# Kernel optimization log

Hardware: AMD Instinct MI355X
Metric: run time of the kernel (lower is better)

Reference implementation:

```python
import jax, jax.numpy as jnp
import numpy as np

EPS = 1e-5
TOPK = 2
SHARED_RATIO = 0.1

B, S, H = 2, 1024, 2048
NH, DH, R = 16, 128, 64
CQ, CKV = 1024, 512
E, I, NS = 8, 1024, 2


def rmsnorm(x, w):
    return x * jax.lax.rsqrt(jnp.mean(x * x, axis=-1, keepdims=True) + EPS) * w


def rope_cos_sin(seq_len, dim):
    inv = 1.0 / (10000.0 ** (jnp.arange(0, dim, 2, dtype=jnp.float32) / dim))
    t = jnp.arange(seq_len, dtype=jnp.float32)[:, None] * inv[None, :]  # [S, dim/2]
    return jnp.cos(t), jnp.sin(t)


def apply_rope(x, cos, sin):
    # rotate-half on last dim; cos/sin broadcast over leading dims
    x1, x2 = jnp.split(x, 2, axis=-1)
    return jnp.concatenate([x1 * cos - x2 * sin, x2 * cos + x1 * sin], axis=-1)


def swiglu(x, w1, w3, w2):
    return (jax.nn.silu(x @ w1) * (x @ w3)) @ w2


def setup_inputs() -> dict:
    key = jax.random.key(0)
    ks = jax.random.split(key, 24)
    sc = 0.02
    d = {
        'x': jax.random.normal(ks[0], (B, S, H), jnp.float32),
        'attn_norm_w': jnp.ones((H,), jnp.float32),
        'ffn_norm_w': jnp.ones((H,), jnp.float32),
        'W_dq': sc * jax.random.normal(ks[1], (H, CQ), jnp.float32),
        'q_norm_w': jnp.ones((CQ,), jnp.float32),
        'W_uq': sc * jax.random.normal(ks[2], (CQ, NH * DH), jnp.float32),
        'W_qr': sc * jax.random.normal(ks[3], (CQ, NH * R), jnp.float32),
        'W_dkv': sc * jax.random.normal(ks[4], (H, CKV), jnp.float32),
        'kv_norm_w': jnp.ones((CKV,), jnp.float32),
        'W_uk': sc * jax.random.normal(ks[5], (CKV, NH * DH), jnp.float32),
        'W_uv': sc * jax.random.normal(ks[6], (CKV, NH * DH), jnp.float32),
        'W_kr': sc * jax.random.normal(ks[7], (H, R), jnp.float32),
        'W_o': sc * jax.random.normal(ks[8], (NH * DH, H), jnp.float32),
        'centroids': sc * jax.random.normal(ks[9], (E, H), jnp.float32),
        'expert_bias': jnp.zeros((E,), jnp.float32),
        'w1': sc * jax.random.normal(ks[10], (E, H, I), jnp.float32),
        'w3': sc * jax.random.normal(ks[11], (E, H, I), jnp.float32),
        'w2': sc * jax.random.normal(ks[12], (E, I, H), jnp.float32),
        'w1s': sc * jax.random.normal(ks[13], (NS, H, I), jnp.float32),
        'w3s': sc * jax.random.normal(ks[14], (NS, H, I), jnp.float32),
        'w2s': sc * jax.random.normal(ks[15], (NS, I, H), jnp.float32),
    }
    return d


def reference(x, attn_norm_w, ffn_norm_w, W_dq, q_norm_w, W_uq, W_qr, W_dkv,
              kv_norm_w, W_uk, W_uv, W_kr, W_o, centroids, expert_bias,
              w1, w3, w2, w1s, w3s, w2s):
    b, s, h = x.shape
    r = W_kr.shape[1]
    nh = W_qr.shape[1] // r
    dh = W_uq.shape[1] // nh

    # ---- MLA attention (pre-norm) ----
    hn = rmsnorm(x, attn_norm_w)
    cq = rmsnorm(hn @ W_dq, q_norm_w)                    # [b,s,CQ] compressed query latent
    q = (cq @ W_uq).reshape(b, s, nh, dh)                # content queries
    qr = (cq @ W_qr).reshape(b, s, nh, r)                # rope queries
    ckv = rmsnorm(hn @ W_dkv, kv_norm_w)                 # [b,s,CKV] compressed kv latent
    k = (ckv @ W_uk).reshape(b, s, nh, dh)
    v = (ckv @ W_uv).reshape(b, s, nh, dh)
    kr = hn @ W_kr                                       # [b,s,r] shared rope key

    cos, sin = rope_cos_sin(s, r)
    qr = apply_rope(qr, cos[None, :, None, :], sin[None, :, None, :])
    kr = apply_rope(kr, cos[None, :, :], sin[None, :, :])

    scale = 1.0 / np.sqrt(dh + r).astype(np.float32)
    scores = (jnp.einsum('bqhd,bkhd->bhqk', q, k)
              + jnp.einsum('bqhr,bkr->bhqk', qr, kr)) * scale
    causal = jnp.tril(jnp.ones((s, s), dtype=bool))
    scores = jnp.where(causal[None, None], scores, jnp.finfo(scores.dtype).min)
    attn = jax.nn.softmax(scores, axis=-1)
    attn_out = jnp.einsum('bhqk,bkhd->bqhd', attn, v).reshape(b, s, nh * dh) @ W_o
    x = x + attn_out

    # ---- aux-loss-free MoE (pre-norm) ----
    h2 = rmsnorm(x, ffn_norm_w).reshape(b * s, h)
    gate_scores = jax.nn.sigmoid(h2 @ centroids.T)       # [T,E]
    _, idx = jax.lax.top_k(gate_scores + expert_bias[None, :], TOPK)  # bias only for selection
    gw = jnp.take_along_axis(gate_scores, idx, axis=1)
    gw = gw / jnp.sum(gw, axis=1, keepdims=True)
    dense_w = jnp.sum(jax.nn.one_hot(idx, gate_scores.shape[1], dtype=h2.dtype) * gw[..., None], axis=1)  # [T,E]

    moe = jnp.zeros_like(h2)
    for e in range(w1.shape[0]):
        moe = moe + dense_w[:, e:e + 1] * swiglu(h2, w1[e], w3[e], w2[e])
    for si in range(w1s.shape[0]):
        moe = moe + SHARED_RATIO * swiglu(h2, w1s[si], w3s[si], w2s[si])

    return x + moe.reshape(b, s, h)
```

## Files before the change

kernel.cpp:

```cpp
#include <hip/hip_runtime.h>
#include <hip/hip_bf16.h>
#include <math.h>

typedef unsigned short u16;
typedef __attribute__((ext_vector_type(8))) short s8v;
typedef __attribute__((ext_vector_type(4))) short s4v;
typedef __attribute__((ext_vector_type(4))) float f4v;

#define B_   2
#define S_   1024
#define T_   2048
#define H_   2048
#define NH_  16
#define DH_  128
#define R_   64
#define CQ_  1024
#define CKV_ 512
#define DQK_ 192
#define E_   8
#define I_   1024
#define NS_  2

__device__ __forceinline__ float us2f(u16 u){
  unsigned int i = ((unsigned int)u) << 16; float f; __builtin_memcpy(&f, &i, 4); return f;
}
__device__ __forceinline__ u16 f2us(float f){
  unsigned int i; __builtin_memcpy(&i, &f, 4);
  unsigned int r = i + 0x7fffu + ((i >> 16) & 1u);
  return (u16)(r >> 16);
}
__device__ __forceinline__ f4v MFMA_B16(s8v a, s8v b, f4v c){
  return __builtin_amdgcn_mfma_f32_16x16x32_bf16(a, b, c, 0, 0, 0);
}

typedef const __attribute__((address_space(1))) void* gas_ptr;
typedef __attribute__((address_space(3))) void* las_ptr;
__device__ __forceinline__ void gload16(const void* g, void* l){
  __builtin_amdgcn_global_load_lds((gas_ptr)g, (las_ptr)l, 16, 0, 0);
}

__global__ void rope_table_kernel(float* __restrict__ cosT, float* __restrict__ sinT){
  int i = blockIdx.x * 256 + threadIdx.x;
  if (i >= S_ * 32) return;
  int s = i >> 5, f = i & 31;
  double inv = exp(-(double)f / 32.0 * log(10000.0));
  double t = (double)s * inv;
  cosT[i] = (float)cos(t);
  sinT[i] = (float)sin(t);
}

__global__ __launch_bounds__(256) void ttc_kernel(const float* __restrict__ in, u16* __restrict__ outp,
                                                  int Kd, int Nd, size_t zs, int rowoff){
  __shared__ float tile[64][65];
  size_t ibase = (size_t)blockIdx.z * Kd * Nd;
  size_t obase = (size_t)blockIdx.z * zs;
  int k0 = blockIdx.y * 64, n0 = blockIdx.x * 64;
  int tid = threadIdx.x;
  int tx = tid & 15, ty = tid >> 4;
  #pragma unroll
  for (int pp = 0; pp < 4; pp++){
    int kk = pp * 16 + ty;
    f4v v = *(const f4v*)(in + ibase + (size_t)(k0 + kk) * Nd + n0 + tx * 4);
    tile[kk][tx * 4 + 0] = v[0];
    tile[kk][tx * 4 + 1] = v[1];
    tile[kk][tx * 4 + 2] = v[2];
    tile[kk][tx * 4 + 3] = v[3];
  }
  __syncthreads();
  #pragma unroll
  for (int pp = 0; pp < 4; pp++){
    int nn = pp * 16 + ty;
    s4v o;
    #pragma unroll
    for (int j = 0; j < 4; j++) o[j] = (short)f2us(tile[tx * 4 + j][nn]);
    *(s4v*)(outp + obase + (size_t)(rowoff + n0 + nn) * Kd + k0 + tx * 4) = o;
  }
}

__global__ __launch_bounds__(256) void rmsnorm_kernel(const float* __restrict__ in, const float* __restrict__ w,
                                                      u16* __restrict__ outb, float* __restrict__ outf, int D){
  int t = blockIdx.x;
  const float* row = in + (size_t)t * D;
  float ss = 0.f;
  for (int i = threadIdx.x * 4; i < D; i += 1024){
    f4v v = *(const f4v*)(row + i);
    ss += v[0]*v[0] + v[1]*v[1] + v[2]*v[2] + v[3]*v[3];
  }
  #pragma unroll
  for (int m = 1; m < 64; m <<= 1) ss += __shfl_xor(ss, m);
  __shared__ float red[4];
  if ((threadIdx.x & 63) == 0) red[threadIdx.x >> 6] = ss;
  __syncthreads();
  float tot = red[0] + red[1] + red[2] + red[3];
  float r = 1.0f / sqrtf(tot / (float)D + 1e-5f);
  for (int i = threadIdx.x * 4; i < D; i += 1024){
    f4v v = *(const f4v*)(row + i);
    f4v wv = *(const f4v*)(w + i);
    s4v ob;
    f4v of;
    #pragma unroll
    for (int j = 0; j < 4; j++){ of[j] = v[j] * r * wv[j]; ob[j] = (short)f2us(of[j]); }
    *(s4v*)(outb + (size_t)t * D + i) = ob;
    if (outf) *(f4v*)(outf + (size_t)t * D + i) = of;
  }
}

template<int OUTMODE, bool AGATHER>
__device__ __forceinline__ void gemm_core(const u16* __restrict__ A, int lda,
                                          const u16* __restrict__ Bt, int K, int M,
                                          const int* __restrict__ arows,
                                          float* __restrict__ outf0, float* __restrict__ outf1,
                                          u16* __restrict__ outb0, u16* __restrict__ outb1,
                                          int ldc0, int ldc1, int split,
                                          const float* __restrict__ resid,
                                          int bm0, int bn0){
  __shared__ u16 As[2][128 * 32];
  __shared__ u16 Bs[2][128 * 32];
  int tid = threadIdx.x;
  int w = tid >> 6, lane = tid & 63;
  int wr = w >> 2, wc = w & 3;
  int g = lane >> 4, l16 = lane & 15;

  f4v acc[4][2];
  #pragma unroll
  for (int m = 0; m < 4; m++)
    #pragma unroll
    for (int n = 0; n < 2; n++) acc[m][n] = (f4v)0.0f;

  int c = tid;
  int row = c >> 2;
  int sc = (c & 3) ^ ((c >> 3) & 3);
  int grow = bm0 + row;
  int ar;
  if (AGATHER) ar = arows[(grow < M) ? grow : 0];
  else         ar = (grow < M) ? grow : 0;
  const u16* asrc = A + (size_t)ar * lda + sc * 8;
  const u16* bsrc = Bt + (size_t)(bn0 + row) * K + sc * 8;
  int dst = (w * 64) * 8;
  int apos = (g ^ ((l16 >> 1) & 3)) * 8;

  int nt = K >> 5;
  gload16(asrc, &As[0][dst]);
  gload16(bsrc, &Bs[0][dst]);
  asm volatile("s_waitcnt vmcnt(0)" ::: "memory");
  __builtin_amdgcn_s_barrier();

  int cur = 0;
  for (int t = 0; t < nt; ++t){
    if (t + 1 < nt){
      int kn = (t + 1) * 32;
      gload16(asrc + kn, &As[cur ^ 1][dst]);
      gload16(bsrc + kn, &Bs[cur ^ 1][dst]);
    }
    s8v af[4], bf[2];
    #pragma unroll
    for (int m = 0; m < 4; m++) af[m] = *(const s8v*)(&As[cur][(wr * 64 + m * 16 + l16) * 32 + apos]);
    #pragma unroll
    for (int n = 0; n < 2; n++) bf[n] = *(const s8v*)(&Bs[cur][(wc * 32 + n * 16 + l16) * 32 + apos]);
    __builtin_amdgcn_s_setprio(1);
    #pragma unroll
    for (int m = 0; m < 4; m++)
      #pragma unroll
      for (int n = 0; n < 2; n++)
        acc[m][n] = MFMA_B16(af[m], bf[n], acc[m][n]);
    __builtin_amdgcn_s_setprio(0);
    if (t + 1 < nt){
      asm volatile("s_waitcnt vmcnt(0)" ::: "memory");
      __builtin_amdgcn_s_barrier();
    }
    cur ^= 1;
  }

  #pragma unroll
  for (int m = 0; m < 4; m++)
    #pragma unroll
    for (int n = 0; n < 2; n++){
      int ccol = bn0 + wc * 32 + n * 16 + l16;
      #pragma unroll
      for (int j = 0; j < 4; j++){
        int r = wr * 64 + m * 16 + g * 4 + j;
        int gr = bm0 + r;
        if (gr >= M) continue;
        float v = acc[m][n][j];
        if (OUTMODE == 0){
          outf0[(size_t)gr * ldc0 + ccol] = v;
        } else if (OUTMODE == 1){
          outb0[(size_t)gr * ldc0 + ccol] = f2us(v);
        } else if (OUTMODE == 2){
          outf0[(size_t)gr * ldc0 + ccol] = v + resid[(size_t)gr * ldc0 + ccol];
        } else if (OUTMODE == 3){
          if (ccol < split) outf0[(size_t)gr * ldc0 + ccol] = v;
          else              outf1[(size_t)gr * ldc1 + (ccol - split)] = v;
        } else {
          if (ccol < split) outb0[(size_t)gr * ldc0 + ccol] = f2us(v);
          else              outb1[(size_t)gr * ldc1 + (ccol - split)] = f2us(v);
        }
      }
    }
}

template<int OUTMODE>
__global__ __launch_bounds__(512) void gemm_kernel(const u16* __restrict__ A, int lda,
                                                   const u16* __restrict__ Bt, int K, int M,
                                                   float* __restrict__ outf0, float* __restrict__ outf1,
                                                   u16* __restrict__ outb0, u16* __restrict__ outb1,
                                                   int ldc0, int ldc1, int split,
                                                   const float* __restrict__ resid){
  int gx = gridDim.x;
  int nwg = gx * gridDim.y;
  int orig = blockIdx.y * gx + blockIdx.x;
  int wg = orig;
  if ((nwg & 7) == 0) wg = (orig & 7) * (nwg >> 3) + (orig >> 3);
  int bx = wg % gx, by = wg / gx;
  gemm_core<OUTMODE, false>(A, lda, Bt, K, M, nullptr,
                            outf0, outf1, outb0, outb1, ldc0, ldc1, split, resid,
                            by * 128, bx * 128);
}

__global__ __launch_bounds__(64) void kr_kernel(const u16* __restrict__ hn, const float* __restrict__ Wkr,
                                                const float* __restrict__ cosT, const float* __restrict__ sinT,
                                                float* __restrict__ krb){
  int t = blockIdx.x, lane = threadIdx.x;
  float acc = 0.f;
  const u16* hrow = hn + (size_t)t * H_;
  for (int k = 0; k < H_; k += 8){
    #pragma unroll
    for (int u = 0; u < 8; u++) acc += us2f(hrow[k + u]) * Wkr[(size_t)(k + u) * R_ + lane];
  }
  float other = __shfl_xor(acc, 32);
  int s = t & (S_ - 1);
  int f = lane & 31;
  float c = cosT[s * 32 + f], sn = sinT[s * 32 + f];
  float v = (lane < 32) ? (acc * c - other * sn) : (acc * c + other * sn);
  krb[(size_t)t * R_ + lane] = v;
}

__global__ void build_qcat_kernel(const u16* __restrict__ qbuf, const u16* __restrict__ qrb,
                                  const float* __restrict__ cosT, const float* __restrict__ sinT,
                                  u16* __restrict__ qcat){
  size_t i = (size_t)blockIdx.x * 256 + threadIdx.x;
  const size_t total = (size_t)B_ * NH_ * S_ * DQK_;
  if (i >= total) return;
  int d = i % DQK_; size_t rem = i / DQK_;
  int s = rem % S_; rem /= S_;
  int h = rem % NH_; int b = rem / NH_;
  int t = b * S_ + s;
  u16 v;
  if (d < DH_) v = qbuf[(size_t)t * H_ + h * DH_ + d];
  else {
    int r = d - DH_;
    int rr = r & 31;
    float c = cosT[s * 32 + rr], sn = sinT[s * 32 + rr];
    float x1 = us2f(qrb[(size_t)t * (NH_ * R_) + h * R_ + rr]);
    float x2 = us2f(qrb[(size_t)t * (NH_ * R_) + h * R_ + rr + 32]);
    float val = (r < 32) ? (x1 * c - x2 * sn) : (x2 * c + x1 * sn);
    v = f2us(val);
  }
  qcat[i] = v;
}

__global__ void build_kcat_kernel(const u16* __restrict__ kbuf, const float* __restrict__ krb,
                                  u16* __restrict__ kcat){
  size_t i = (size_t)blockIdx.x * 256 + threadIdx.x;
  const size_t total = (size_t)B_ * NH_ * S_ * DQK_;
  if (i >= total) return;
  int d = i % DQK_; size_t rem = i / DQK_;
  int s = rem % S_; rem /= S_;
  int h = rem % NH_; int b = rem / NH_;
  int t = b * S_ + s;
  u16 v;
  if (d < DH_) v = kbuf[(size_t)t * H_ + h * DH_ + d];
  else v = f2us(krb[(size_t)t * R_ + (d - DH_)]);
  kcat[i] = v;
}

__global__ __launch_bounds__(256) void build_vT_kernel(const u16* __restrict__ vbuf, u16* __restrict__ vT){
  __shared__ u16 tile[32][33];
  int bh = blockIdx.z; int b = bh >> 4, h = bh & 15;
  int s0 = blockIdx.x * 32, d0 = blockIdx.y * 32;
  int tx = threadIdx.x & 31, ty = threadIdx.x >> 5;
  for (int i = ty; i < 32; i += 8)
    tile[i][tx] = vbuf[(size_t)(b * S_ + s0 + i) * H_ + h * DH_ + d0 + tx];
  __syncthreads();
  for (int i = ty; i < 32; i += 8)
    vT[((size_t)bh * DH_ + d0 + i) * S_ + s0 + tx] = tile[tx][i];
}

__global__ __launch_bounds__(256) void attn_kernel(const u16* __restrict__ qcat, const u16* __restrict__ kcat,
                                                   const u16* __restrict__ vT, u16* __restrict__ aout){
  __shared__ u16 Ks[64 * 192];
  __shared__ u16 Vs[128 * 64];
  __shared__ u16 Ps[4][16][72];

  int qb = (int)(gridDim.x - 1) - (int)blockIdx.x;
  int h = blockIdx.y, b = blockIdx.z;
  int bh = b * NH_ + h;
  int tid = threadIdx.x;
  int w = tid >> 6, lane = tid & 63;
  int g = lane >> 4, l16 = lane & 15;
  int qrow0 = qb * 64 + w * 16;
  int qglob = qrow0 + l16;
  int qmax = qrow0 + 15;
  const float scale = 0.07216878364870323f;

  s8v qf[6];
  const u16* qrow = qcat + ((size_t)bh * S_ + qglob) * DQK_;
  #pragma unroll
  for (int c = 0; c < 6; c++) qf[c] = *(const s8v*)(qrow + c * 32 + g * 8);

  int koff[6];
  #pragma unroll
  for (int i = 0; i < 6; i++){
    int ci = tid + i * 256;
    int row = ci / 24, cp = ci - row * 24;
    koff[i] = row * 192 + ((cp ^ (row & 7)) * 8);
  }
  int voff[4];
  #pragma unroll
  for (int i = 0; i < 4; i++){
    int ci = tid + i * 256;
    int d = ci >> 3, cp = ci & 7;
    voff[i] = d * S_ + ((cp ^ (d & 7)) * 8);
  }

  const u16* kbase_g = kcat + (size_t)bh * S_ * DQK_;
  const u16* vbase_g = vT + (size_t)bh * DH_ * S_;

  f4v o[8];
  #pragma unroll
  for (int i = 0; i < 8; i++) o[i] = (f4v)0.0f;
  float mrow = -1e30f, lrow = 0.0f;

  int nkt = qb + 1;
  for (int it = 0; it < nkt; it++){
    int kv0 = it * 64;
    const u16* ksrc = kbase_g + (size_t)kv0 * DQK_;
    #pragma unroll
    for (int i = 0; i < 6; i++) gload16(ksrc + koff[i], &Ks[(i * 256 + w * 64) * 8]);
    #pragma unroll
    for (int i = 0; i < 4; i++) gload16(vbase_g + kv0 + voff[i], &Vs[(i * 256 + w * 64) * 8]);
    __syncthreads();

    f4v st[4];
    #pragma unroll
    for (int kf = 0; kf < 4; kf++){
      f4v a = (f4v)0.0f;
      if (kv0 + kf * 16 <= qmax){
        int row = kf * 16 + l16;
        int sw = (row & 7);
        #pragma unroll
        for (int c = 0; c < 6; c++){
          s8v kfr = *(const s8v*)(&Ks[row * 192 + (((c * 4 + g) ^ sw) * 8)]);
          a = MFMA_B16(kfr, qf[c], a);
        }
      }
      st[kf] = a;
    }

    float sv[16];
    #pragma unroll
    for (int kf = 0; kf < 4; kf++)
      #pragma unroll
      for (int j = 0; j < 4; j++){
        int kk = kv0 + kf * 16 + g * 4 + j;
        sv[kf * 4 + j] = (kk <= qglob) ? st[kf][j] * scale : -1e30f;
      }

    float mt = sv[0];
    #pragma unroll
    for (int i = 1; i < 16; i++) mt = fmaxf(mt, sv[i]);
    mt = fmaxf(mt, __shfl_xor(mt, 16));
    mt = fmaxf(mt, __shfl_xor(mt, 32));
    float mnew = fmaxf(mrow, mt);
    float corr = __expf(mrow - mnew);
    float ps = 0.f;
    u16 pb[16];
    #pragma unroll
    for (int i = 0; i < 16; i++){ float pv = __expf(sv[i] - mnew); ps += pv; pb[i] = f2us(pv); }
    ps += __shfl_xor(ps, 16); ps += __shfl_xor(ps, 32);
    lrow = lrow * corr + ps;
    mrow = mnew;
    #pragma unroll
    for (int i = 0; i < 8; i++) o[i] *= corr;

    #pragma unroll
    for (int kf = 0; kf < 4; kf++){
      s4v pw;
      #pragma unroll
      for (int j = 0; j < 4; j++) pw[j] = (short)pb[kf * 4 + j];
      *(s4v*)(&Ps[w][l16][kf * 16 + g * 4]) = pw;
    }

    #pragma unroll
    for (int ks = 0; ks < 2; ks++){
      if (kv0 + ks * 32 <= qmax){
        s4v plo = *(const s4v*)(&Ps[w][l16][ks * 32 + g * 8]);
        s4v phi = *(const s4v*)(&Ps[w][l16][ks * 32 + g * 8 + 4]);
        s8v pf;
        pf[0] = plo[0]; pf[1] = plo[1]; pf[2] = plo[2]; pf[3] = plo[3];
        pf[4] = phi[0]; pf[5] = phi[1]; pf[6] = phi[2]; pf[7] = phi[3];
        #pragma unroll
        for (int dt = 0; dt < 8; dt++){
          int d = dt * 16 + l16;
          s8v vf = *(const s8v*)(&Vs[d * 64 + ((((ks * 4 + g) ^ (d & 7))) * 8)]);
          o[dt] = MFMA_B16(vf, pf, o[dt]);
        }
      }
    }
    __syncthreads();
  }

  float inv = 1.0f / lrow;
  int trow = b * S_ + qglob;
  #pragma unroll
  for (int dt = 0; dt < 8; dt++){
    s4v wv;
    #pragma unroll
    for (int j = 0; j < 4; j++) wv[j] = (short)f2us(o[dt][j] * inv);
    *(s4v*)(aout + (size_t)trow * H_ + h * DH_ + dt * 16 + g * 4) = wv;
  }
}

__global__ __launch_bounds__(64) void route_kernel(const float* __restrict__ h2f, const float* __restrict__ cent,
                                                   const float* __restrict__ bias,
                                                   int* __restrict__ eidx, float* __restrict__ ew,
                                                   int* __restrict__ counts){
  int t = blockIdx.x, lane = threadIdx.x;
  float acc[E_];
  #pragma unroll
  for (int e = 0; e < E_; e++) acc[e] = 0.f;
  for (int k = lane; k < H_; k += 64){
    float xv = h2f[(size_t)t * H_ + k];
    #pragma unroll
    for (int e = 0; e < E_; e++) acc[e] += xv * cent[(size_t)e * H_ + k];
  }
  #pragma unroll
  for (int m = 1; m < 64; m <<= 1)
    #pragma unroll
    for (int e = 0; e < E_; e++) acc[e] += __shfl_xor(acc[e], m);
  float s[E_], sb[E_];
  #pragma unroll
  for (int e = 0; e < E_; e++){ s[e] = 1.f / (1.f + expf(-acc[e])); sb[e] = s[e] + bias[e]; }
  int i0 = 0;
  #pragma unroll
  for (int e = 1; e < E_; e++) if (sb[e] > sb[i0]) i0 = e;
  int i1 = -1;
  #pragma unroll
  for (int e = 0; e < E_; e++) if (e != i0 && (i1 < 0 || sb[e] > sb[i1])) i1 = e;
  float w0 = s[i0], w1 = s[i1], nrm = w0 + w1;
  w0 /= nrm; w1 /= nrm;
  if (lane == 0){
    eidx[t * 2] = i0; eidx[t * 2 + 1] = i1;
    ew[t * 2] = w0; ew[t * 2 + 1] = w1;
    atomicAdd(&counts[i0], 1); atomicAdd(&counts[i1], 1);
  }
}

__global__ void scan_kernel(int* __restrict__ meta){
  if (threadIdx.x == 0 && blockIdx.x == 0){
    int off = 0;
    for (int e = 0; e < E_; e++){ meta[16 + e] = off; meta[32 + e] = meta[e]; off += meta[e]; }
    meta[16 + 8] = 4096; meta[32 + 8] = T_;
    meta[16 + 9] = 4096 + T_; meta[32 + 9] = T_;
  }
}

__global__ void fill_kernel(const int* __restrict__ eidx, const float* __restrict__ ew,
                            int* __restrict__ meta, int* __restrict__ rowlist, float* __restrict__ roww,
                            int* __restrict__ slotidx){
  int t = blockIdx.x * 256 + threadIdx.x;
  if (t >= T_) return;
  for (int j = 0; j < 2; j++){
    int e = eidx[t * 2 + j];
    int p = atomicAdd(&meta[8 + e], 1);
    int slot = meta[16 + e] + p;
    rowlist[slot] = t; roww[slot] = ew[t * 2 + j];
    slotidx[t * 2 + j] = slot;
  }
}

__global__ void init_shared_kernel(int* __restrict__ rowlist, float* __restrict__ roww){
  int i = blockIdx.x * 256 + threadIdx.x;
  if (i >= 2 * T_) return;
  rowlist[4096 + i] = i & (T_ - 1);
  roww[4096 + i] = 0.1f;
}

__global__ __launch_bounds__(512) void moe_gemm13_kernel(const u16* __restrict__ h2b,
    const u16* __restrict__ w13T, const u16* __restrict__ w13sT,
    const int* __restrict__ rowlist, const int* __restrict__ listoff, const int* __restrict__ cnt2,
    u16* __restrict__ t1b, u16* __restrict__ t3b){
  int e = blockIdx.z;
  int cnt = cnt2[e];
  if ((int)(blockIdx.y * 128) >= cnt) return;
  const u16* Bt = (e < 8) ? w13T + (size_t)e * 2048 * H_ : w13sT + (size_t)(e - 8) * 2048 * H_;
  int loff = listoff[e];
  gemm_core<4, true>(h2b, H_, Bt, H_, cnt, rowlist + loff,
                     nullptr, nullptr, t1b + (size_t)loff * I_, t3b + (size_t)loff * I_,
                     I_, I_, 1024, nullptr,
                     blockIdx.y * 128, blockIdx.x * 128);
}

__global__ __launch_bounds__(512) void moe_gemm2_kernel(const u16* __restrict__ ub,
    const u16* __restrict__ w2T, const u16* __restrict__ w2sT,
    const int* __restrict__ listoff, const int* __restrict__ cnt2,
    u16* __restrict__ o2){
  int e = blockIdx.z;
  int cnt = cnt2[e];
  if ((int)(blockIdx.y * 128) >= cnt) return;
  const u16* Bt = (e < 8) ? w2T + (size_t)e * H_ * I_ : w2sT + (size_t)(e - 8) * H_ * I_;
  int loff = listoff[e];
  gemm_core<1, false>(ub + (size_t)loff * I_, I_, Bt, I_, cnt, nullptr,
                      nullptr, nullptr, o2 + (size_t)loff * H_, nullptr,
                      H_, 0, 0, nullptr,
                      blockIdx.y * 128, blockIdx.x * 128);
}

__global__ __launch_bounds__(256) void silumul_kernel(const u16* __restrict__ t1b, const u16* __restrict__ t3b,
                                                      const float* __restrict__ roww, u16* __restrict__ ub){
  size_t i = ((size_t)blockIdx.x * 256 + threadIdx.x) * 8;
  if (i >= (size_t)8192 * I_) return;
  int row = (int)(i / I_);
  float w = roww[row];
  s8v a = *(const s8v*)(t1b + i);
  s8v b = *(const s8v*)(t3b + i);
  s8v o;
  #pragma unroll
  for (int j = 0; j < 8; j++){
    float av = us2f((u16)a[j]);
    float gm = av / (1.f + __expf(-av));
    o[j] = (short)f2us(gm * us2f((u16)b[j]) * w);
  }
  *(s8v*)(ub + i) = o;
}

__global__ __launch_bounds__(256) void combine_kernel(const float* __restrict__ x1, const u16* __restrict__ o2,
                                                      const int* __restrict__ slotidx, float* __restrict__ out){
  int t = blockIdx.x;
  int s0 = slotidx[2 * t], s1 = slotidx[2 * t + 1];
  const u16* r0 = o2 + (size_t)s0 * H_;
  const u16* r1 = o2 + (size_t)s1 * H_;
  const u16* r2 = o2 + (size_t)(4096 + t) * H_;
  const u16* r3 = o2 + (size_t)(4096 + T_ + t) * H_;
  const float* rx = x1 + (size_t)t * H_;
  float* ro = out + (size_t)t * H_;
  int c = threadIdx.x * 8;
  s8v v0 = *(const s8v*)(r0 + c);
  s8v v1 = *(const s8v*)(r1 + c);
  s8v v2 = *(const s8v*)(r2 + c);
  s8v v3 = *(const s8v*)(r3 + c);
  #pragma unroll
  for (int j = 0; j < 8; j++){
    ro[c + j] = rx[c + j] + us2f((u16)v0[j]) + us2f((u16)v1[j]) + us2f((u16)v2[j]) + us2f((u16)v3[j]);
  }
}

extern "C" void kernel_launch(void* const* d_in, const int* in_sizes, int n_in,
                              void* d_out, int out_size, void* d_ws, size_t ws_size,
                              hipStream_t stream){
  const float* x    = (const float*)d_in[0];
  const float* anw  = (const float*)d_in[1];
  const float* fnw  = (const float*)d_in[2];
  const float* Wdq  = (const float*)d_in[3];
  const float* qnw  = (const float*)d_in[4];
  const float* Wuq  = (const float*)d_in[5];
  const float* Wqr  = (const float*)d_in[6];
  const float* Wdkv = (const float*)d_in[7];
  const float* kvnw = (const float*)d_in[8];
  const float* Wuk  = (const float*)d_in[9];
  const float* Wuv  = (const float*)d_in[10];
  const float* Wkr  = (const float*)d_in[11];
  const float* Wo   = (const float*)d_in[12];
  const float* cent = (const float*)d_in[13];
  const float* ebias= (const float*)d_in[14];
  const float* w1   = (const float*)d_in[15];
  const float* w3   = (const float*)d_in[16];
  const float* w2   = (const float*)d_in[17];
  const float* w1s  = (const float*)d_in[18];
  const float* w3s  = (const float*)d_in[19];
  const float* w2s  = (const float*)d_in[20];
  float* out = (float*)d_out;

  char* p = (char*)d_ws;
  auto alloc = [&](size_t bytes)->void*{
    void* r = (void*)p; p += (bytes + 255) & ~(size_t)255; return r;
  };

  float* cosT = (float*)alloc((size_t)S_ * 32 * 4);
  float* sinT = (float*)alloc((size_t)S_ * 32 * 4);
  u16* WdqkvT = (u16*)alloc((size_t)1536 * H_ * 2);
  u16* WuqrT  = (u16*)alloc((size_t)3072 * CQ_ * 2);
  u16* WukvT  = (u16*)alloc((size_t)4096 * CKV_ * 2);
  u16* WoT   = (u16*)alloc((size_t)H_ * H_ * 2);
  u16* w13T  = (u16*)alloc((size_t)E_ * 2048 * H_ * 2);
  u16* w2T   = (u16*)alloc((size_t)E_ * H_ * I_ * 2);
  u16* w13sT = (u16*)alloc((size_t)NS_ * 2048 * H_ * 2);
  u16* w2sT  = (u16*)alloc((size_t)NS_ * H_ * I_ * 2);
  float* x1  = (float*)alloc((size_t)T_ * H_ * 4);
  float* h2f = (float*)alloc((size_t)T_ * H_ * 4);
  u16* h2b   = (u16*)alloc((size_t)T_ * H_ * 2);
  int* meta  = (int*)alloc(64 * 4);
  int* eidx  = (int*)alloc((size_t)T_ * 2 * 4);
  float* ew  = (float*)alloc((size_t)T_ * 2 * 4);
  int* rowlist = (int*)alloc(8192 * 4);
  float* roww  = (float*)alloc(8192 * 4);
  int* slotidx = (int*)alloc((size_t)T_ * 2 * 4);

  char* mark = p;
  u16* hn    = (u16*)alloc((size_t)T_ * H_ * 2);
  float* tq  = (float*)alloc((size_t)T_ * CQ_ * 4);
  u16* cq    = (u16*)alloc((size_t)T_ * CQ_ * 2);
  u16* qbuf  = (u16*)alloc((size_t)T_ * H_ * 2);
  u16* qrb   = (u16*)alloc((size_t)T_ * NH_ * R_ * 2);
  float* tkv = (float*)alloc((size_t)T_ * CKV_ * 4);
  u16* ckv   = (u16*)alloc((size_t)T_ * CKV_ * 2);
  u16* kbuf  = (u16*)alloc((size_t)T_ * H_ * 2);
  u16* vbuf  = (u16*)alloc((size_t)T_ * H_ * 2);
  float* krb = (float*)alloc((size_t)T_ * R_ * 4);
  u16* qcat  = (u16*)alloc((size_t)B_ * NH_ * S_ * DQK_ * 2);
  u16* kcat  = (u16*)alloc((size_t)B_ * NH_ * S_ * DQK_ * 2);
  u16* vT    = (u16*)alloc((size_t)B_ * NH_ * DH_ * S_ * 2);
  u16* aout  = (u16*)alloc((size_t)T_ * H_ * 2);

  p = mark;
  u16* t1b = (u16*)alloc((size_t)8192 * I_ * 2);
  u16* t3b = (u16*)alloc((size_t)8192 * I_ * 2);
  u16* ub  = (u16*)alloc((size_t)8192 * I_ * 2);
  u16* o2  = (u16*)alloc((size_t)8192 * H_ * 2);

  dim3 b256(256), b64(64), b512(512);

  hipMemsetAsync(meta, 0, 64 * 4, stream);

  rope_table_kernel<<<dim3((S_ * 32 + 255) / 256), b256, 0, stream>>>(cosT, sinT);

  ttc_kernel<<<dim3(CQ_ / 64, H_ / 64, 1),  b256, 0, stream>>>(Wdq,  WdqkvT, H_,  CQ_, 0, 0);
  ttc_kernel<<<dim3(CKV_ / 64, H_ / 64, 1), b256, 0, stream>>>(Wdkv, WdqkvT, H_,  CKV_, 0, 1024);
  ttc_kernel<<<dim3(H_ / 64, CQ_ / 64, 1),  b256, 0, stream>>>(Wuq,  WuqrT,  CQ_, H_, 0, 0);
  ttc_kernel<<<dim3(1024 / 64, CQ_ / 64, 1), b256, 0, stream>>>(Wqr, WuqrT,  CQ_, 1024, 0, 2048);
  ttc_kernel<<<dim3(H_ / 64, CKV_ / 64, 1), b256, 0, stream>>>(Wuk,  WukvT,  CKV_, H_, 0, 0);
  ttc_kernel<<<dim3(H_ / 64, CKV_ / 64, 1), b256, 0, stream>>>(Wuv,  WukvT,  CKV_, H_, 0, 2048);
  ttc_kernel<<<dim3(H_ / 64, H_ / 64, 1),   b256, 0, stream>>>(Wo,   WoT,    H_,  H_, 0, 0);
  ttc_kernel<<<dim3(I_ / 64, H_ / 64, E_),  b256, 0, stream>>>(w1,  w13T, H_, I_, (size_t)2048 * H_, 0);
  ttc_kernel<<<dim3(I_ / 64, H_ / 64, E_),  b256, 0, stream>>>(w3,  w13T, H_, I_, (size_t)2048 * H_, 1024);
  ttc_kernel<<<dim3(H_ / 64, I_ / 64, E_),  b256, 0, stream>>>(w2,  w2T,  I_, H_, (size_t)H_ * I_, 0);
  ttc_kernel<<<dim3(I_ / 64, H_ / 64, NS_), b256, 0, stream>>>(w1s, w13sT, H_, I_, (size_t)2048 * H_, 0);
  ttc_kernel<<<dim3(I_ / 64, H_ / 64, NS_), b256, 0, stream>>>(w3s, w13sT, H_, I_, (size_t)2048 * H_, 1024);
  ttc_kernel<<<dim3(H_ / 64, I_ / 64, NS_), b256, 0, stream>>>(w2s, w2sT, I_, H_, (size_t)H_ * I_, 0);

  rmsnorm_kernel<<<T_, b256, 0, stream>>>(x, anw, hn, nullptr, H_);

  gemm_kernel<3><<<dim3(1536 / 128, T_ / 128), b512, 0, stream>>>(hn, H_, WdqkvT, H_, T_,
      tq, tkv, nullptr, nullptr, CQ_, CKV_, 1024, nullptr);
  rmsnorm_kernel<<<T_, b256, 0, stream>>>(tq, qnw, cq, nullptr, CQ_);
  rmsnorm_kernel<<<T_, b256, 0, stream>>>(tkv, kvnw, ckv, nullptr, CKV_);
  gemm_kernel<4><<<dim3(3072 / 128, T_ / 128), b512, 0, stream>>>(cq, CQ_, WuqrT, CQ_, T_,
      nullptr, nullptr, qbuf, qrb, H_, NH_ * R_, 2048, nullptr);
  gemm_kernel<4><<<dim3(4096 / 128, T_ / 128), b512, 0, stream>>>(ckv, CKV_, WukvT, CKV_, T_,
      nullptr, nullptr, kbuf, vbuf, H_, H_, 2048, nullptr);
  kr_kernel<<<T_, b64, 0, stream>>>(hn, Wkr, cosT, sinT, krb);

  size_t qct = (size_t)B_ * NH_ * S_ * DQK_;
  build_qcat_kernel<<<dim3((qct + 255) / 256), b256, 0, stream>>>(qbuf, qrb, cosT, sinT, qcat);
  build_kcat_kernel<<<dim3((qct + 255) / 256), b256, 0, stream>>>(kbuf, krb, kcat);
  build_vT_kernel<<<dim3(S_ / 32, DH_ / 32, B_ * NH_), b256, 0, stream>>>(vbuf, vT);

  attn_kernel<<<dim3(S_ / 64, NH_, B_), b256, 0, stream>>>(qcat, kcat, vT, aout);

  gemm_kernel<2><<<dim3(H_ / 128, T_ / 128), b512, 0, stream>>>(aout, H_, WoT, H_, T_,
      x1, nullptr, nullptr, nullptr, H_, 0, 0, x);

  rmsnorm_kernel<<<T_, b256, 0, stream>>>(x1, fnw, h2b, h2f, H_);
  route_kernel<<<T_, b64, 0, stream>>>(h2f, cent, ebias, eidx, ew, meta);
  scan_kernel<<<dim3(1), b64, 0, stream>>>(meta);
  fill_kernel<<<dim3((T_ + 255) / 256), b256, 0, stream>>>(eidx, ew, meta, rowlist, roww, slotidx);
  init_shared_kernel<<<dim3((2 * T_ + 255) / 256), b256, 0, stream>>>(rowlist, roww);

  moe_gemm13_kernel<<<dim3(2048 / 128, 16, 10), b512, 0, stream>>>(h2b, w13T, w13sT,
      rowlist, meta + 16, meta + 32, t1b, t3b);
  silumul_kernel<<<dim3((8192 * I_ / 8 + 255) / 256), b256, 0, stream>>>(t1b, t3b, roww, ub);
  moe_gemm2_kernel<<<dim3(H_ / 128, 16, 10), b512, 0, stream>>>(ub, w2T, w2sT,
      meta + 16, meta + 32, o2);

  combine_kernel<<<T_, b256, 0, stream>>>(x1, o2, slotidx, out);
}
```

Baseline: 699.2 us.

## Fuse k_rope projection into down-projection GEMM, vectorize cat builders, restructure pipeline

The separate scalar kr_kernel, which computed the rope key projection with one 64-thread block per token, is removed. W_kr is instead transposed into extra rows of the combined down-projection weight, so the main GEMM writes the unrotated kr directly. The rope rotation moves into build_kcat, and build_qcat and build_kcat now process 8 elements per thread with vector stores. The GEMM main loop also changes its wait and barrier placement, using vmcnt(2) with barriers at both ends of each iteration, which adds a barrier per step but allows partial overlap of loads.

```diff
diff --git a/kernel.cpp b/kernel.cpp
--- a/kernel.cpp
+++ b/kernel.cpp
@@ -110,8 +110,9 @@
                                           const u16* __restrict__ Bt, int K, int M,
                                           const int* __restrict__ arows,
                                           float* __restrict__ outf0, float* __restrict__ outf1,
+                                          float* __restrict__ outf2,
                                           u16* __restrict__ outb0, u16* __restrict__ outb1,
-                                          int ldc0, int ldc1, int split,
+                                          int ldc0, int ldc1, int split, int split2,
                                           const float* __restrict__ resid,
                                           int bm0, int bn0){
   __shared__ u16 As[2][128 * 32];
@@ -142,8 +143,6 @@
   int nt = K >> 5;
   gload16(asrc, &As[0][dst]);
   gload16(bsrc, &Bs[0][dst]);
-  asm volatile("s_waitcnt vmcnt(0)" ::: "memory");
-  __builtin_amdgcn_s_barrier();
 
   int cur = 0;
   for (int t = 0; t < nt; ++t){
@@ -151,7 +150,12 @@
       int kn = (t + 1) * 32;
       gload16(asrc + kn, &As[cur ^ 1][dst]);
       gload16(bsrc + kn, &Bs[cur ^ 1][dst]);
+      asm volatile("s_waitcnt vmcnt(2)" ::: "memory");
+    } else {
+      asm volatile("s_waitcnt vmcnt(0)" ::: "memory");
     }
+    __builtin_amdgcn_s_barrier();
+    asm volatile("" ::: "memory");
     s8v af[4], bf[2];
     #pragma unroll
     for (int m = 0; m < 4; m++) af[m] = *(const s8v*)(&As[cur][(wr * 64 + m * 16 + l16) * 32 + apos]);
@@ -164,10 +168,8 @@
       for (int n = 0; n < 2; n++)
         acc[m][n] = MFMA_B16(af[m], bf[n], acc[m][n]);
     __builtin_amdgcn_s_setprio(0);
-    if (t + 1 < nt){
-      asm volatile("s_waitcnt vmcnt(0)" ::: "memory");
-      __builtin_amdgcn_s_barrier();
-    }
+    asm volatile("" ::: "memory");
+    __builtin_amdgcn_s_barrier();
     cur ^= 1;
   }
 
@@ -188,12 +190,13 @@
           outb0[(size_t)gr * ldc0 + ccol] = f2us(v);
         } else if (OUTMODE == 2){
           outf0[(size_t)gr * ldc0 + ccol] = v + resid[(size_t)gr * ldc0 + ccol];
-        } else if (OUTMODE == 3){
-          if (ccol < split) outf0[(size_t)gr * ldc0 + ccol] = v;
-          else              outf1[(size_t)gr * ldc1 + (ccol - split)] = v;
-        } else {
+        } else if (OUTMODE == 4){
           if (ccol < split) outb0[(size_t)gr * ldc0 + ccol] = f2us(v);
           else              outb1[(size_t)gr * ldc1 + (ccol - split)] = f2us(v);
+        } else {
+          if (ccol < split)       outf0[(size_t)gr * ldc0 + ccol] = v;
+          else if (ccol < split2) outf1[(size_t)gr * ldc1 + (ccol - split)] = v;
+          else if (ccol < split2 + 64) outf2[(size_t)gr * 64 + (ccol - split2)] = v;
         }
       }
     }
@@ -203,8 +206,9 @@
 __global__ __launch_bounds__(512) void gemm_kernel(const u16* __restrict__ A, int lda,
                                                    const u16* __restrict__ Bt, int K, int M,
                                                    float* __restrict__ outf0, float* __restrict__ outf1,
+                                                   float* __restrict__ outf2,
                                                    u16* __restrict__ outb0, u16* __restrict__ outb1,
-                                                   int ldc0, int ldc1, int split,
+                                                   int ldc0, int ldc1, int split, int split2,
                                                    const float* __restrict__ resid){
   int gx = gridDim.x;
   int nwg = gx * gridDim.y;
@@ -213,65 +217,64 @@
   if ((nwg & 7) == 0) wg = (orig & 7) * (nwg >> 3) + (orig >> 3);
   int bx = wg % gx, by = wg / gx;
   gemm_core<OUTMODE, false>(A, lda, Bt, K, M, nullptr,
-                            outf0, outf1, outb0, outb1, ldc0, ldc1, split, resid,
+                            outf0, outf1, outf2, outb0, outb1, ldc0, ldc1, split, split2, resid,
                             by * 128, bx * 128);
 }
 
-__global__ __launch_bounds__(64) void kr_kernel(const u16* __restrict__ hn, const float* __restrict__ Wkr,
-                                                const float* __restrict__ cosT, const float* __restrict__ sinT,
-                                                float* __restrict__ krb){
-  int t = blockIdx.x, lane = threadIdx.x;
-  float acc = 0.f;
-  const u16* hrow = hn + (size_t)t * H_;
-  for (int k = 0; k < H_; k += 8){
-    #pragma unroll
-    for (int u = 0; u < 8; u++) acc += us2f(hrow[k + u]) * Wkr[(size_t)(k + u) * R_ + lane];
-  }
-  float other = __shfl_xor(acc, 32);
-  int s = t & (S_ - 1);
-  int f = lane & 31;
-  float c = cosT[s * 32 + f], sn = sinT[s * 32 + f];
-  float v = (lane < 32) ? (acc * c - other * sn) : (acc * c + other * sn);
-  krb[(size_t)t * R_ + lane] = v;
-}
-
-__global__ void build_qcat_kernel(const u16* __restrict__ qbuf, const u16* __restrict__ qrb,
-                                  const float* __restrict__ cosT, const float* __restrict__ sinT,
-                                  u16* __restrict__ qcat){
-  size_t i = (size_t)blockIdx.x * 256 + threadIdx.x;
+__global__ __launch_bounds__(256) void build_qcat_kernel(const u16* __restrict__ qbuf, const u16* __restrict__ qrb,
+                                                         const float* __restrict__ cosT, const float* __restrict__ sinT,
+                                                         u16* __restrict__ qcat){
+  size_t i8 = ((size_t)blockIdx.x * 256 + threadIdx.x) * 8;
   const size_t total = (size_t)B_ * NH_ * S_ * DQK_;
-  if (i >= total) return;
-  int d = i % DQK_; size_t rem = i / DQK_;
-  int s = rem % S_; rem /= S_;
-  int h = rem % NH_; int b = rem / NH_;
+  if (i8 >= total) return;
+  int d = (int)(i8 % DQK_); size_t rem = i8 / DQK_;
+  int s = (int)(rem % S_); rem /= S_;
+  int h = (int)(rem % NH_); int b = (int)(rem / NH_);
   int t = b * S_ + s;
-  u16 v;
-  if (d < DH_) v = qbuf[(size_t)t * H_ + h * DH_ + d];
-  else {
-    int r = d - DH_;
-    int rr = r & 31;
-    float c = cosT[s * 32 + rr], sn = sinT[s * 32 + rr];
-    float x1 = us2f(qrb[(size_t)t * (NH_ * R_) + h * R_ + rr]);
-    float x2 = us2f(qrb[(size_t)t * (NH_ * R_) + h * R_ + rr + 32]);
-    float val = (r < 32) ? (x1 * c - x2 * sn) : (x2 * c + x1 * sn);
-    v = f2us(val);
-  }
-  qcat[i] = v;
-}
-
-__global__ void build_kcat_kernel(const u16* __restrict__ kbuf, const float* __restrict__ krb,
-                                  u16* __restrict__ kcat){
-  size_t i = (size_t)blockIdx.x * 256 + threadIdx.x;
+  s8v o;
+  if (d < DH_){
+    o = *(const s8v*)(qbuf + (size_t)t * H_ + h * DH_ + d);
+  } else {
+    int r0 = d - DH_;
+    int rr0 = r0 & 31;
+    const u16* qp = qrb + (size_t)t * (NH_ * R_) + h * R_;
+    #pragma unroll
+    for (int j = 0; j < 8; j++){
+      float c = cosT[s * 32 + rr0 + j], sn = sinT[s * 32 + rr0 + j];
+      float lo = us2f(qp[rr0 + j]), hi = us2f(qp[rr0 + 32 + j]);
+      float val = (r0 < 32) ? (lo * c - hi * sn) : (hi * c + lo * sn);
+      o[j] = (short)f2us(val);
+    }
+  }
+  *(s8v*)(qcat + i8) = o;
+}
+
+__global__ __launch_bounds__(256) void build_kcat_kernel(const u16* __restrict__ kbuf, const float* __restrict__ krb,
+                                                         const float* __restrict__ cosT, const float* __restrict__ sinT,
+                                                         u16* __restrict__ kcat){
+  size_t i8 = ((size_t)blockIdx.x * 256 + threadIdx.x) * 8;
   const size_t total = (size_t)B_ * NH_ * S_ * DQK_;
-  if (i >= total) return;
-  int d = i % DQK_; size_t rem = i / DQK_;
-  int s = rem % S_; rem /= S_;
-  int h = rem % NH_; int b = rem / NH_;
+  if (i8 >= total) return;
+  int d = (int)(i8 % DQK_); size_t rem = i8 / DQK_;
+  int s = (int)(rem % S_); rem /= S_;
+  int h = (int)(rem % NH_); int b = (int)(rem / NH_);
   int t = b * S_ + s;
-  u16 v;
-  if (d < DH_) v = kbuf[(size_t)t * H_ + h * DH_ + d];
-  else v = f2us(krb[(size_t)t * R_ + (d - DH_)]);
-  kcat[i] = v;
+  s8v o;
+  if (d < DH_){
+    o = *(const s8v*)(kbuf + (size_t)t * H_ + h * DH_ + d);
+  } else {
+    int r0 = d - DH_;
+    int rr0 = r0 & 31;
+    const float* kp = krb + (size_t)t * R_;
+    #pragma unroll
+    for (int j = 0; j < 8; j++){
+      float c = cosT[s * 32 + rr0 + j], sn = sinT[s * 32 + rr0 + j];
+      float lo = kp[rr0 + j], hi = kp[rr0 + 32 + j];
+      float val = (r0 < 32) ? (lo * c - hi * sn) : (hi * c + lo * sn);
+      o[j] = (short)f2us(val);
+    }
+  }
+  *(s8v*)(kcat + i8) = o;
 }
 
 __global__ __launch_bounds__(256) void build_vT_kernel(const u16* __restrict__ vbuf, u16* __restrict__ vT){
@@ -496,8 +499,8 @@
   const u16* Bt = (e < 8) ? w13T + (size_t)e * 2048 * H_ : w13sT + (size_t)(e - 8) * 2048 * H_;
   int loff = listoff[e];
   gemm_core<4, true>(h2b, H_, Bt, H_, cnt, rowlist + loff,
-                     nullptr, nullptr, t1b + (size_t)loff * I_, t3b + (size_t)loff * I_,
-                     I_, I_, 1024, nullptr,
+                     nullptr, nullptr, nullptr, t1b + (size_t)loff * I_, t3b + (size_t)loff * I_,
+                     I_, I_, 1024, 0, nullptr,
                      blockIdx.y * 128, blockIdx.x * 128);
 }
 
@@ -511,8 +514,8 @@
   const u16* Bt = (e < 8) ? w2T + (size_t)e * H_ * I_ : w2sT + (size_t)(e - 8) * H_ * I_;
   int loff = listoff[e];
   gemm_core<1, false>(ub + (size_t)loff * I_, I_, Bt, I_, cnt, nullptr,
-                      nullptr, nullptr, o2 + (size_t)loff * H_, nullptr,
-                      H_, 0, 0, nullptr,
+                      nullptr, nullptr, nullptr, o2 + (size_t)loff * H_, nullptr,
+                      H_, 0, 0, 0, nullptr,
                       blockIdx.y * 128, blockIdx.x * 128);
 }
 
@@ -588,7 +591,7 @@
 
   float* cosT = (float*)alloc((size_t)S_ * 32 * 4);
   float* sinT = (float*)alloc((size_t)S_ * 32 * 4);
-  u16* WdqkvT = (u16*)alloc((size_t)1536 * H_ * 2);
+  u16* WdqkvT = (u16*)alloc((size_t)1664 * H_ * 2);
   u16* WuqrT  = (u16*)alloc((size_t)3072 * CQ_ * 2);
   u16* WukvT  = (u16*)alloc((size_t)4096 * CKV_ * 2);
   u16* WoT   = (u16*)alloc((size_t)H_ * H_ * 2);
@@ -631,11 +634,13 @@
   dim3 b256(256), b64(64), b512(512);
 
   hipMemsetAsync(meta, 0, 64 * 4, stream);
+  hipMemsetAsync(WdqkvT + (size_t)1600 * H_, 0, (size_t)64 * H_ * 2, stream);
 
   rope_table_kernel<<<dim3((S_ * 32 + 255) / 256), b256, 0, stream>>>(cosT, sinT);
 
   ttc_kernel<<<dim3(CQ_ / 64, H_ / 64, 1),  b256, 0, stream>>>(Wdq,  WdqkvT, H_,  CQ_, 0, 0);
   ttc_kernel<<<dim3(CKV_ / 64, H_ / 64, 1), b256, 0, stream>>>(Wdkv, WdqkvT, H_,  CKV_, 0, 1024);
+  ttc_kernel<<<dim3(1, H_ / 64, 1),         b256, 0, stream>>>(Wkr,  WdqkvT, H_,  R_, 0, 1536);
   ttc_kernel<<<dim3(H_ / 64, CQ_ / 64, 1),  b256, 0, stream>>>(Wuq,  WuqrT,  CQ_, H_, 0, 0);
   ttc_kernel<<<dim3(1024 / 64, CQ_ / 64, 1), b256, 0, stream>>>(Wqr, WuqrT,  CQ_, 1024, 0, 2048);
   ttc_kernel<<<dim3(H_ / 64, CKV_ / 64, 1), b256, 0, stream>>>(Wuk,  WukvT,  CKV_, H_, 0, 0);
@@ -650,25 +655,24 @@
 
   rmsnorm_kernel<<<T_, b256, 0, stream>>>(x, anw, hn, nullptr, H_);
 
-  gemm_kernel<3><<<dim3(1536 / 128, T_ / 128), b512, 0, stream>>>(hn, H_, WdqkvT, H_, T_,
-      tq, tkv, nullptr, nullptr, CQ_, CKV_, 1024, nullptr);
+  gemm_kernel<5><<<dim3(1664 / 128, T_ / 128), b512, 0, stream>>>(hn, H_, WdqkvT, H_, T_,
+      tq, tkv, krb, nullptr, nullptr, CQ_, CKV_, 1024, 1536, nullptr);
   rmsnorm_kernel<<<T_, b256, 0, stream>>>(tq, qnw, cq, nullptr, CQ_);
   rmsnorm_kernel<<<T_, b256, 0, stream>>>(tkv, kvnw, ckv, nullptr, CKV_);
   gemm_kernel<4><<<dim3(3072 / 128, T_ / 128), b512, 0, stream>>>(cq, CQ_, WuqrT, CQ_, T_,
-      nullptr, nullptr, qbuf, qrb, H_, NH_ * R_, 2048, nullptr);
+      nullptr, nullptr, nullptr, qbuf, qrb, H_, NH_ * R_, 2048, 0, nullptr);
   gemm_kernel<4><<<dim3(4096 / 128, T_ / 128), b512, 0, stream>>>(ckv, CKV_, WukvT, CKV_, T_,
-      nullptr, nullptr, kbuf, vbuf, H_, H_, 2048, nullptr);
-  kr_kernel<<<T_, b64, 0, stream>>>(hn, Wkr, cosT, sinT, krb);
+      nullptr, nullptr, nullptr, kbuf, vbuf, H_, H_, 2048, 0, nullptr);
 
   size_t qct = (size_t)B_ * NH_ * S_ * DQK_;
-  build_qcat_kernel<<<dim3((qct + 255) / 256), b256, 0, stream>>>(qbuf, qrb, cosT, sinT, qcat);
-  build_kcat_kernel<<<dim3((qct + 255) / 256), b256, 0, stream>>>(kbuf, krb, kcat);
+  build_qcat_kernel<<<dim3((qct / 8 + 255) / 256), b256, 0, stream>>>(qbuf, qrb, cosT, sinT, qcat);
+  build_kcat_kernel<<<dim3((qct / 8 + 255) / 256), b256, 0, stream>>>(kbuf, krb, cosT, sinT, kcat);
   build_vT_kernel<<<dim3(S_ / 32, DH_ / 32, B_ * NH_), b256, 0, stream>>>(vbuf, vT);
 
   attn_kernel<<<dim3(S_ / 64, NH_, B_), b256, 0, stream>>>(qcat, kcat, vT, aout);
 
   gemm_kernel<2><<<dim3(H_ / 128, T_ / 128), b512, 0, stream>>>(aout, H_, WoT, H_, T_,
-      x1, nullptr, nullptr, nullptr, H_, 0, 0, x);
+      x1, nullptr, nullptr, nullptr, nullptr, H_, 0, 0, 0, x);
 
   rmsnorm_kernel<<<T_, b256, 0, stream>>>(x1, fnw, h2b, h2f, H_);
   route_kernel<<<T_, b64, 0, stream>>>(h2f, cent, ebias, eidx, ew, meta);
```

Result: faster. 633.2 us (-9.4%).
